# Optimization experiments

Measured on AMD Instinct MI355X. Metric: run time of the kernel, lower is better.

Reference implementation:

```python
import jax, jax.numpy as jnp
import numpy as np

N = 131072      # points (rays x samples chunk)
E = 8           # spatial sub-networks (centroids)
DIN = 90        # encoded pos+dir features fed to sub-NeRFs (xyz_real=True -> x[:, 3:])
H = 256         # sub-NeRF hidden width
DOUT = 4        # rgb + sigma
MARGIN = 2.0    # boundary_margin
EPS = 1e-8


def setup_inputs() -> dict:
    key = jax.random.key(0)
    k = jax.random.split(key, 5)
    x_xyz = jax.random.uniform(k[0], (N, 3), dtype=jnp.float32)          # routing coords in [0,1)^3
    x_feat = jax.random.normal(k[1], (N, DIN), dtype=jnp.float32)        # encoded features
    x = jnp.concatenate([x_xyz, x_feat], axis=1)                         # [N, 3+DIN]
    centroids = jax.random.uniform(k[2], (E, 3), dtype=jnp.float32)
    W1 = jax.random.normal(k[3], (E, DIN, H), dtype=jnp.float32) * 0.05
    b1 = jnp.zeros((E, H), dtype=jnp.float32)
    W2 = jax.random.normal(k[4], (E, H, DOUT), dtype=jnp.float32) * 0.05
    b2 = jnp.zeros((E, DOUT), dtype=jnp.float32)
    return {"x": x, "centroids": centroids, "W1": W1, "b1": b1, "W2": W2, "b2": b2}


def reference(x, centroids, W1, b1, W2, b2):
    # --- centroid routing (torch.cdist equivalent) ---
    xyz = x[:, :3]                                                       # [N,3]
    d2 = jnp.sum((xyz[:, None, :] - centroids[None, :, :]) ** 2, axis=-1)
    dist = jnp.sqrt(jnp.maximum(d2, 0.0))                                # [N,E]
    inv = 1.0 / (dist + EPS)
    min_d = jnp.min(dist, axis=1, keepdims=True)                         # [N,1]
    inv = jnp.where(dist > MARGIN * min_d, 0.0, inv)                     # zero far experts
    weights = inv / jnp.sum(inv, axis=-1, keepdims=True)                 # [N,E], rows sum to 1

    # --- per-expert sub-NeRF MLP, weighted combine ---
    # Dense-equivalent of masked gather + weighted scatter-add: experts whose
    # weight is exactly 0 contribute nothing, matching the torch masked path.
    feat = x[:, 3:]                                                      # xyz_real=True -> drop xyz
    h = jax.nn.relu(jnp.einsum('nd,edh->enh', feat, W1) + b1[:, None, :])  # [E,N,H]
    out_e = jnp.einsum('enh,eho->eno', h, W2) + b2[:, None, :]             # [E,N,DOUT]
    return jnp.einsum('eno,ne->no', out_e, weights)                        # [N,DOUT]
```

## Files before the change

kernel.cpp:

```cpp
#include <hip/hip_runtime.h>

#define NPTS 131072
#define NE 8
#define DIN 90
#define NH 256

typedef __attribute__((ext_vector_type(8))) short bf16x8;
typedef __attribute__((ext_vector_type(4))) float f32x4;
typedef __attribute__((ext_vector_type(2))) float f32x2;
typedef __attribute__((ext_vector_type(4))) unsigned int u32x4;
typedef __attribute__((ext_vector_type(2))) unsigned int u32x2;
typedef __attribute__((ext_vector_type(4), aligned(4))) float f32x4a;
typedef __attribute__((ext_vector_type(2), aligned(4))) float f32x2a;

__device__ __forceinline__ unsigned short f2bf(float f) {
  unsigned int u = __float_as_uint(f);
  u += 0x7fffu + ((u >> 16) & 1u);
  return (unsigned short)(u >> 16);
}

#if defined(__has_builtin) && __has_builtin(__builtin_amdgcn_cvt_pk_bf16_f32)
typedef __attribute__((ext_vector_type(2))) __bf16 bf16x2;
__device__ __forceinline__ unsigned int pkbf(float f0, float f1) {
  bf16x2 r = __builtin_amdgcn_cvt_pk_bf16_f32(f0, f1);
  return __builtin_bit_cast(unsigned int, r);
}
#else
__device__ __forceinline__ unsigned int pkbf(float f0, float f1) {
  unsigned int u0 = __float_as_uint(f0) + 0x7fffu;
  unsigned int u1 = __float_as_uint(f1) + 0x7fffu;
  return __builtin_amdgcn_perm(u1, u0, 0x07060302u);
}
#endif

__device__ __forceinline__ bf16x8 cvt8(f32x4 a, f32x4 b) {
  u32x4 r;
  r[0] = pkbf(a[0], a[1]);
  r[1] = pkbf(a[2], a[3]);
  r[2] = pkbf(b[0], b[1]);
  r[3] = pkbf(b[2], b[3]);
  return __builtin_bit_cast(bf16x8, r);
}

#define PREP_T (184320 + 12288 + 8192 + 24576)
__global__ __launch_bounds__(256) void prep(const float* __restrict__ W1,
                                            const float* __restrict__ W2,
                                            unsigned short* __restrict__ W1T,
                                            unsigned short* __restrict__ W2T) {
  int tid = blockIdx.x * 256 + threadIdx.x;
  if (tid < 184320) {
    float v = W1[tid];
    int n = tid & 255, r = tid >> 8;
    int kp = r % 90, e = r / 90;
    W1T[(size_t)(e * NH + n) * 96 + kp] = f2bf(v);
    return;
  }
  tid -= 184320;
  if (tid < 12288) {
    int kp = 90 + tid % 6, q = tid / 6;
    int n = q & 255, e = q >> 8;
    W1T[(size_t)(e * NH + n) * 96 + kp] = 0;
    return;
  }
  tid -= 12288;
  if (tid < 8192) {
    float v = W2[tid];
    int o = tid & 3, k = (tid >> 2) & 255, e = tid >> 10;
    W2T[(size_t)(e * 16 + o) * NH + k] = f2bf(v);
    return;
  }
  tid -= 8192;
  if (tid < 24576) {
    int k = tid & 255, q = tid >> 8;
    int o = 4 + q % 12, e = q / 12;
    W2T[(size_t)(e * 16 + o) * NH + k] = 0;
  }
}

__global__ __launch_bounds__(256, 3) void meganerf_main(
    const float* __restrict__ x, const float* __restrict__ cent,
    const float* __restrict__ b1, const float* __restrict__ b2,
    const unsigned short* __restrict__ W1T, const unsigned short* __restrict__ W2T,
    float* __restrict__ out) {
  __shared__ unsigned short sH[4 * 2048];
  __shared__ float sW[NE][64];
  __shared__ float sB2[64][4];
  __shared__ float sB1[NE * NH];

  const int t    = threadIdx.x;
  const int lane = t & 63;
  const int wid  = t >> 6;
  const int l15  = lane & 15;
  const int l4   = lane >> 4;
  const int row0 = blockIdx.x * 64;
  const int gbase = wid * 2048;

#pragma unroll
  for (int j = 0; j < 2; ++j)
    *(f32x4*)&sB1[t * 4 + j * 1024] = *(const f32x4a*)&b1[t * 4 + j * 1024];

  bf16x8 bfr[4][3];
#pragma unroll
  for (int nf = 0; nf < 4; ++nf) {
    const float* gr = x + (size_t)(row0 + 16 * nf + l15) * 93 + 3;
    f32x4 v0, v1;
    v0 = *(const f32x4a*)(gr + 8 * l4);
    v1 = *(const f32x4a*)(gr + 8 * l4 + 4);
    bfr[nf][0] = cvt8(v0, v1);
    v0 = *(const f32x4a*)(gr + 32 + 8 * l4);
    v1 = *(const f32x4a*)(gr + 36 + 8 * l4);
    bfr[nf][1] = cvt8(v0, v1);
    if (l4 < 3) {
      v0 = *(const f32x4a*)(gr + 64 + 8 * l4);
      v1 = *(const f32x4a*)(gr + 68 + 8 * l4);
    } else {
      f32x2 tl = *(const f32x2a*)(gr + 88);
      v0[0] = tl[0]; v0[1] = tl[1]; v0[2] = 0.f; v0[3] = 0.f;
      v1[0] = 0.f; v1[1] = 0.f; v1[2] = 0.f; v1[3] = 0.f;
    }
    bfr[nf][2] = cvt8(v0, v1);
  }

  if (t < 64) {
    const float* gx = x + (size_t)(row0 + t) * 93;
    float px = gx[0], py = gx[1], pz = gx[2];
    float dist[NE], inv[NE];
    float mind = 3.4e38f;
#pragma unroll
    for (int e = 0; e < NE; ++e) {
      float dx = px - cent[e * 3 + 0];
      float dy = py - cent[e * 3 + 1];
      float dz = pz - cent[e * 3 + 2];
      float d2 = dx * dx + dy * dy + dz * dz;
      float d = sqrtf(fmaxf(d2, 0.f));
      dist[e] = d;
      inv[e] = 1.f / (d + 1e-8f);
      mind = fminf(mind, d);
    }
    float s = 0.f;
#pragma unroll
    for (int e = 0; e < NE; ++e) {
      if (dist[e] > 2.0f * mind) inv[e] = 0.f;
      s += inv[e];
    }
    float rs = 1.f / s;
    float bb[4] = {0.f, 0.f, 0.f, 0.f};
#pragma unroll
    for (int e = 0; e < NE; ++e) {
      float w = inv[e] * rs;
      sW[e][t] = w;
#pragma unroll
      for (int o = 0; o < 4; ++o) bb[o] += w * b2[e * 4 + o];
    }
#pragma unroll
    for (int o = 0; o < 4; ++o) sB2[t][o] = bb[o];
  }
  __syncthreads();

  bf16x8 w1buf[2][6];
  bf16x8 bwbuf[2];
  float wv[4];

  auto loadW1 = [&](int idx, int buf) {
    const int e = idx >> 1, c = idx & 1;
    const unsigned short* p =
        W1T + (size_t)(e * NH + 128 * c + 32 * wid + l15) * 96 + 8 * l4;
#pragma unroll
    for (int mf = 0; mf < 2; ++mf)
#pragma unroll
      for (int ks = 0; ks < 3; ++ks)
        w1buf[buf][mf * 3 + ks] = *(const bf16x8*)(p + mf * (16 * 96) + 32 * ks);
  };
  auto loadBW = [&](int idx, int buf) {
    const int e = idx >> 1, c = idx & 1;
    bwbuf[buf] = *(const bf16x8*)(W2T + (size_t)(e * 16 + l15) * NH +
                                  128 * c + 32 * wid + 8 * l4);
  };

  loadBW(0, 0);
  loadW1(0, 0);

  f32x4 facc[4] = {{0.f, 0.f, 0.f, 0.f}, {0.f, 0.f, 0.f, 0.f},
                   {0.f, 0.f, 0.f, 0.f}, {0.f, 0.f, 0.f, 0.f}};

#pragma unroll 2
  for (int i = 0; i < 16; ++i) {
    const int e = i >> 1, c = i & 1, cur = i & 1, nxt = cur ^ 1;
    const int colbase = 128 * c + 32 * wid;

    f32x4 b1v0 = *(const f32x4*)&sB1[e * NH + colbase + 4 * l4];
    f32x4 b1v1 = *(const f32x4*)&sB1[e * NH + colbase + 16 + 4 * l4];
    if (c == 0) {
#pragma unroll
      for (int nf = 0; nf < 4; ++nf) wv[nf] = sW[e][16 * nf + l15];
    }

    const int ip = (i + 1) & 15;
    loadBW(ip, nxt);
    loadW1(ip, nxt);

#pragma unroll
    for (int mf = 0; mf < 2; ++mf) {
      const f32x4 b1v = (mf == 0) ? b1v0 : b1v1;
      f32x4 acc[4];
#pragma unroll
      for (int nf = 0; nf < 4; ++nf)
        acc[nf] = __builtin_amdgcn_mfma_f32_16x16x32_bf16(
            w1buf[cur][mf * 3 + 0], bfr[nf][0], b1v, 0, 0, 0);
#pragma unroll
      for (int ks = 1; ks < 3; ++ks)
#pragma unroll
        for (int nf = 0; nf < 4; ++nf)
          acc[nf] = __builtin_amdgcn_mfma_f32_16x16x32_bf16(
              w1buf[cur][mf * 3 + ks], bfr[nf][ks], acc[nf], 0, 0, 0);

#pragma unroll
      for (int nf = 0; nf < 4; ++nf) {
        const float w = wv[nf];
        f32x4 a = acc[nf];
        f32x2 p0, p1;
        p0[0] = a[0]; p0[1] = a[1];
        p1[0] = a[2]; p1[1] = a[3];
        const f32x2 z = {0.f, 0.f};
        p0 = __builtin_elementwise_max(p0, z) * w;
        p1 = __builtin_elementwise_max(p1, z) * w;
        u32x2 pk;
        pk[0] = pkbf(p0[0], p0[1]);
        pk[1] = pkbf(p1[0], p1[1]);
        *(u32x2*)&sH[gbase + (nf * 64 + (l15 + 16 * (2 * mf + (l4 >> 1)))) * 8 +
                     4 * (l4 & 1)] = pk;
      }
    }

#pragma unroll
    for (int rf = 0; rf < 4; ++rf) {
      bf16x8 ah = *(const bf16x8*)&sH[gbase + (rf * 64 + lane) * 8];
      facc[rf] = __builtin_amdgcn_mfma_f32_16x16x32_bf16(ah, bwbuf[cur], facc[rf], 0, 0, 0);
    }
  }

  __syncthreads();
  float* sOutP = (float*)sH;
  if (l15 < 4) {
#pragma unroll
    for (int rf = 0; rf < 4; ++rf)
#pragma unroll
      for (int r = 0; r < 4; ++r)
        sOutP[(wid * 64 + 16 * rf + 4 * l4 + r) * 4 + l15] = facc[rf][r];
  }
  __syncthreads();
  {
    const int row = t >> 2, o = t & 3;
    float v = sB2[row][o] + sOutP[(0 * 64 + row) * 4 + o] + sOutP[(1 * 64 + row) * 4 + o] +
              sOutP[(2 * 64 + row) * 4 + o] + sOutP[(3 * 64 + row) * 4 + o];
    out[row0 * 4 + t] = v;
  }
}

extern "C" void kernel_launch(void* const* d_in, const int* in_sizes, int n_in,
                              void* d_out, int out_size, void* d_ws, size_t ws_size,
                              hipStream_t stream) {
  const float* x    = (const float*)d_in[0];
  const float* cent = (const float*)d_in[1];
  const float* W1   = (const float*)d_in[2];
  const float* b1   = (const float*)d_in[3];
  const float* W2   = (const float*)d_in[4];
  const float* b2   = (const float*)d_in[5];
  float* out = (float*)d_out;

  unsigned short* W1T = (unsigned short*)d_ws;
  unsigned short* W2T = W1T + NE * NH * 96;

  prep<<<(PREP_T + 255) / 256, 256, 0, stream>>>(W1, W2, W1T, W2T);
  meganerf_main<<<NPTS / 64, 256, 0, stream>>>(x, cent, b1, b2, W1T, W2T, out);
}
```

Measured before the change: 163.7 us.

## Software-pipeline second GEMM one step behind and coalesce weight prep via LDS

```diff
diff --git a/kernel.cpp b/kernel.cpp
--- a/kernel.cpp
+++ b/kernel.cpp
@@ -42,38 +42,54 @@
   return __builtin_bit_cast(bf16x8, r);
 }
 
-#define PREP_T (184320 + 12288 + 8192 + 24576)
 __global__ __launch_bounds__(256) void prep(const float* __restrict__ W1,
                                             const float* __restrict__ W2,
                                             unsigned short* __restrict__ W1T,
                                             unsigned short* __restrict__ W2T) {
-  int tid = blockIdx.x * 256 + threadIdx.x;
-  if (tid < 184320) {
-    float v = W1[tid];
-    int n = tid & 255, r = tid >> 8;
-    int kp = r % 90, e = r / 90;
-    W1T[(size_t)(e * NH + n) * 96 + kp] = f2bf(v);
-    return;
-  }
-  tid -= 184320;
-  if (tid < 12288) {
-    int kp = 90 + tid % 6, q = tid / 6;
-    int n = q & 255, e = q >> 8;
-    W1T[(size_t)(e * NH + n) * 96 + kp] = 0;
-    return;
-  }
-  tid -= 12288;
-  if (tid < 8192) {
-    float v = W2[tid];
-    int o = tid & 3, k = (tid >> 2) & 255, e = tid >> 10;
-    W2T[(size_t)(e * 16 + o) * NH + k] = f2bf(v);
-    return;
-  }
-  tid -= 8192;
-  if (tid < 24576) {
-    int k = tid & 255, q = tid >> 8;
-    int o = 4 + q % 12, e = q / 12;
-    W2T[(size_t)(e * 16 + o) * NH + k] = 0;
+  const int t = threadIdx.x;
+  if (blockIdx.x < 32) {
+    const int e = blockIdx.x >> 2;
+    const int n0 = (blockIdx.x & 3) * 64;
+    __shared__ unsigned int ld[64][49];
+    const int nl = t & 63;
+    const int kq = t >> 6;
+#pragma unroll
+    for (int j = 0; j < 12; ++j) {
+      const int kp2 = kq + 4 * j;
+      const int k0 = 2 * kp2, k1 = k0 + 1;
+      unsigned int lo = 0, hi = 0;
+      if (k0 < DIN) lo = f2bf(W1[((size_t)e * DIN + k0) * NH + n0 + nl]);
+      if (k1 < DIN) hi = f2bf(W1[((size_t)e * DIN + k1) * NH + n0 + nl]);
+      ld[nl][kp2] = lo | (hi << 16);
+    }
+    __syncthreads();
+    unsigned int* dst = (unsigned int*)(W1T + (size_t)(e * NH + n0) * 96);
+#pragma unroll
+    for (int j = 0; j < 12; ++j) {
+      const int u = t + 256 * j;
+      dst[u] = ld[u / 48][u % 48];
+    }
+  } else {
+    __shared__ unsigned short lw[4][264];
+    unsigned int* dst = (unsigned int*)W2T;
+    for (int e = 0; e < NE; ++e) {
+#pragma unroll
+      for (int j = 0; j < 4; ++j) {
+        const int idx = t + 256 * j;
+        lw[idx & 3][idx >> 2] = f2bf(W2[(size_t)e * 1024 + idx]);
+      }
+      __syncthreads();
+#pragma unroll
+      for (int j = 0; j < 8; ++j) {
+        const int u = t + 256 * j;
+        const int o = u >> 7, kp = u & 127;
+        unsigned int v = 0;
+        if (o < 4)
+          v = (unsigned int)lw[o][2 * kp] | ((unsigned int)lw[o][2 * kp + 1] << 16);
+        dst[(size_t)e * 2048 + u] = v;
+      }
+      __syncthreads();
+    }
   }
 }
 
@@ -98,6 +114,10 @@
 #pragma unroll
   for (int j = 0; j < 2; ++j)
     *(f32x4*)&sB1[t * 4 + j * 1024] = *(const f32x4a*)&b1[t * 4 + j * 1024];
+
+#pragma unroll
+  for (int j = 0; j < 4; ++j)
+    *(u32x4*)&sH[gbase + (j * 64 + lane) * 8] = (u32x4){0u, 0u, 0u, 0u};
 
   bf16x8 bfr[4][3];
 #pragma unroll
@@ -159,6 +179,7 @@
 
   bf16x8 w1buf[2][6];
   bf16x8 bwbuf[2];
+  bf16x8 bwprev = __builtin_bit_cast(bf16x8, (u32x4){0u, 0u, 0u, 0u});
   float wv[4];
 
   auto loadW1 = [&](int idx, int buf) {
@@ -190,6 +211,12 @@
 
     f32x4 b1v0 = *(const f32x4*)&sB1[e * NH + colbase + 4 * l4];
     f32x4 b1v1 = *(const f32x4*)&sB1[e * NH + colbase + 16 + 4 * l4];
+
+    bf16x8 ah0 = *(const bf16x8*)&sH[gbase + (0 * 64 + lane) * 8];
+    bf16x8 ah1 = *(const bf16x8*)&sH[gbase + (1 * 64 + lane) * 8];
+    bf16x8 ah2 = *(const bf16x8*)&sH[gbase + (2 * 64 + lane) * 8];
+    bf16x8 ah3 = *(const bf16x8*)&sH[gbase + (3 * 64 + lane) * 8];
+
     if (c == 0) {
 #pragma unroll
       for (int nf = 0; nf < 4; ++nf) wv[nf] = sW[e][16 * nf + l15];
@@ -232,11 +259,18 @@
       }
     }
 
-#pragma unroll
-    for (int rf = 0; rf < 4; ++rf) {
-      bf16x8 ah = *(const bf16x8*)&sH[gbase + (rf * 64 + lane) * 8];
-      facc[rf] = __builtin_amdgcn_mfma_f32_16x16x32_bf16(ah, bwbuf[cur], facc[rf], 0, 0, 0);
-    }
+    facc[0] = __builtin_amdgcn_mfma_f32_16x16x32_bf16(ah0, bwprev, facc[0], 0, 0, 0);
+    facc[1] = __builtin_amdgcn_mfma_f32_16x16x32_bf16(ah1, bwprev, facc[1], 0, 0, 0);
+    facc[2] = __builtin_amdgcn_mfma_f32_16x16x32_bf16(ah2, bwprev, facc[2], 0, 0, 0);
+    facc[3] = __builtin_amdgcn_mfma_f32_16x16x32_bf16(ah3, bwprev, facc[3], 0, 0, 0);
+
+    bwprev = bwbuf[cur];
+  }
+
+#pragma unroll
+  for (int rf = 0; rf < 4; ++rf) {
+    bf16x8 ahf = *(const bf16x8*)&sH[gbase + (rf * 64 + lane) * 8];
+    facc[rf] = __builtin_amdgcn_mfma_f32_16x16x32_bf16(ahf, bwprev, facc[rf], 0, 0, 0);
   }
 
   __syncthreads();
@@ -271,6 +305,6 @@
   unsigned short* W1T = (unsigned short*)d_ws;
   unsigned short* W2T = W1T + NE * NH * 96;
 
-  prep<<<(PREP_T + 255) / 256, 256, 0, stream>>>(W1, W2, W1T, W2T);
+  prep<<<33, 256, 0, stream>>>(W1, W2, W1T, W2T);
   meganerf_main<<<NPTS / 64, 256, 0, stream>>>(x, cent, b1, b2, W1T, W2T, out);
 }
```

New measurement: 174.0 us. 6.3% more time.
